# Kernel tuning notes

Measured on AMD Instinct MI355X. Metric: run time of the kernel, lower is better.

## Reference

```python
import jax, jax.numpy as jnp
import numpy as np

N = 50000
E = 800000
F_IN = 256
F_OUT = 128
ALPHA = 0.2  # leaky relu negative slope


def setup_inputs() -> dict:
    key = jax.random.key(0)
    k1, k2, k3, k4 = jax.random.split(key, 4)
    x = jax.random.normal(k1, (N, F_IN), dtype=jnp.float32)
    edge_index = jax.random.randint(k2, (2, E), 0, N, dtype=jnp.int64 if jax.config.jax_enable_x64 else jnp.int32)
    # xavier_normal gain=1.414
    W = jax.random.normal(k3, (F_IN, F_OUT), dtype=jnp.float32) * (1.414 * np.sqrt(2.0 / (F_IN + F_OUT)))
    a = jax.random.normal(k4, (2 * F_OUT, 2 * F_OUT), dtype=jnp.float32) * (1.414 * np.sqrt(2.0 / (4 * F_OUT)))
    return {"x": x, "edge_index": edge_index, "W": W, "a": a}


def reference(x, edge_index, W, a):
    n = x.shape[0]
    src = edge_index[0]  # rows of sparse adj
    dst = edge_index[1]  # cols of sparse adj
    h = x @ W  # [N, F_out]
    hs = h[src]  # [E, F_out] gather
    hd = h[dst]  # [E, F_out] gather
    # att_type == 'mx':
    # (a @ edge_h).sum(0) == a.sum(0) @ edge_h where edge_h = cat(hs, hd).T
    asum = a.sum(0)  # [2*F_out]
    lin = hs @ asum[:F_OUT] + hd @ asum[F_OUT:]  # [E]
    conv = (hs * hd).sum(axis=1)  # [E]
    z = lin * jax.nn.sigmoid(conv)
    edge_e = jnp.exp(-jnp.where(z >= 0, z, ALPHA * z))  # exp(-leakyrelu(z))
    # sparse spmm: rowsum (a @ ones) and aggregate (a @ h); dropout p=0 (eval)
    e_rowsum = jax.ops.segment_sum(edge_e, src, num_segments=n) + 1e-8  # [N]
    h_prime = jax.ops.segment_sum(edge_e[:, None] * hd, src, num_segments=n)  # [N, F_out]
    h_prime = h_prime / e_rowsum[:, None]
    return jax.nn.elu(h_prime)  # concat=True
```

## Files before the change

### kernel.cpp

```cpp
#include <hip/hip_runtime.h>

#define NF_IN 256
#define NF 128
#define NEG_SLOPE 0.2f
#define BUCKET 64

typedef float f32x4 __attribute__((ext_vector_type(4)));
typedef __bf16 bf16x8 __attribute__((ext_vector_type(8)));
typedef short short8 __attribute__((ext_vector_type(8)));
typedef _Float16 half8 __attribute__((ext_vector_type(8)));

__device__ __forceinline__ short bf16_rtne(float f) {
    unsigned u = __float_as_uint(f);
    u += 0x7fffu + ((u >> 16) & 1u);
    return (short)(u >> 16);
}

__global__ __launch_bounds__(256) void stage_pre(const float* __restrict__ a,
                                                 const float* __restrict__ W,
                                                 float* __restrict__ av,
                                                 short* __restrict__ Wt) {
    const int tid = threadIdx.x;
    if (blockIdx.x < 8) {
        float s = 0.f;
        const int r0 = blockIdx.x * 32;
        for (int i = 0; i < 32; ++i) s += a[(size_t)(r0 + i) * (2 * NF) + tid];
        atomicAdd(&av[tid], s);
    } else {
        const int i = (blockIdx.x - 8) * 256 + tid;
        const int k = i >> 7, c = i & 127;
        const int t = k >> 5, lg = (k >> 3) & 3, e = k & 7;
        const int q = c >> 4, col = c & 15;
        const float w = W[i];
        const unsigned b = __float_as_uint(w);
        const int base = t * 8192 + q * 512 + lg * 128 + col * 8 + e;
        Wt[base] = (short)(b >> 16);
        Wt[base + 4096] = bf16_rtne(w - __uint_as_float(b & 0xffff0000u));
    }
}

__global__ __launch_bounds__(256) void stage_proj(const float* __restrict__ x,
                                                  const short* __restrict__ Wt,
                                                  const float* __restrict__ av,
                                                  _Float16* __restrict__ h16,
                                                  float* __restrict__ scs,
                                                  float* __restrict__ scd, int n) {
    __shared__ short bts[2][8192];

    const int tid = threadIdx.x;
    const int lane = tid & 63;
    const int wv = tid >> 6;
    const int l15 = lane & 15;
    const int lg = lane >> 4;
    const int rbase = blockIdx.x * 64 + wv * 16;

    int arow = rbase + l15;
    if (arow >= n) arow = n - 1;
    const float* xr = x + (size_t)arow * NF_IN + lg * 8;

    short8 ah[8], al[8];
    #pragma unroll
    for (int t = 0; t < 8; ++t) {
        const float4 u0 = *(const float4*)(xr + t * 32);
        const float4 u1 = *(const float4*)(xr + t * 32 + 4);
        const float xs[8] = {u0.x, u0.y, u0.z, u0.w, u1.x, u1.y, u1.z, u1.w};
        #pragma unroll
        for (int e = 0; e < 8; ++e) {
            const unsigned b = __float_as_uint(xs[e]);
            ah[t][e] = (short)(b >> 16);
            al[t][e] = bf16_rtne(xs[e] - __uint_as_float(b & 0xffff0000u));
        }
    }

    f32x4 acc[8];
    #pragma unroll
    for (int q = 0; q < 8; ++q) acc[q] = (f32x4){0.f, 0.f, 0.f, 0.f};

    #define STAGE(t_, b_)                                                        \
        do {                                                                     \
            const short* gt_ = Wt + (size_t)(t_) * 8192;                         \
            _Pragma("unroll")                                                    \
            for (int i_ = 0; i_ < 4; ++i_) {                                     \
                const int ch_ = wv * 256 + i_ * 64;                              \
                __builtin_amdgcn_global_load_lds(                                \
                    (const __attribute__((address_space(1))) void*)              \
                        (gt_ + (size_t)(ch_ + lane) * 8),                        \
                    (__attribute__((address_space(3))) void*)&bts[b_][ch_ * 8],  \
                    16, 0, 0);                                                   \
            }                                                                    \
        } while (0)

    STAGE(0, 0);

    #pragma unroll
    for (int t = 0; t < 8; ++t) {
        __syncthreads();
        if (t < 7) STAGE(t + 1, (t + 1) & 1);
        const short* Bs = &bts[t & 1][0];
        const int boff = lg * 128 + l15 * 8;
        const bf16x8 ahv = __builtin_bit_cast(bf16x8, ah[t]);
        const bf16x8 alv = __builtin_bit_cast(bf16x8, al[t]);
        #pragma unroll
        for (int q = 0; q < 8; ++q) {
            const short8 bh = *(const short8*)(Bs + q * 512 + boff);
            const short8 bl = *(const short8*)(Bs + 4096 + q * 512 + boff);
            const bf16x8 bhv = __builtin_bit_cast(bf16x8, bh);
            const bf16x8 blv = __builtin_bit_cast(bf16x8, bl);
            acc[q] = __builtin_amdgcn_mfma_f32_16x16x32_bf16(ahv, bhv, acc[q], 0, 0, 0);
            acc[q] = __builtin_amdgcn_mfma_f32_16x16x32_bf16(alv, bhv, acc[q], 0, 0, 0);
            acc[q] = __builtin_amdgcn_mfma_f32_16x16x32_bf16(ahv, blv, acc[q], 0, 0, 0);
        }
    }
    #undef STAGE

    float avA[8], avB[8];
    #pragma unroll
    for (int q = 0; q < 8; ++q) {
        avA[q] = av[q * 16 + l15];
        avB[q] = av[NF + q * 16 + l15];
    }

    #pragma unroll
    for (int r = 0; r < 4; ++r) {
        float ps = 0.f, pd = 0.f;
        #pragma unroll
        for (int q = 0; q < 8; ++q) {
            ps += acc[q][r] * avA[q];
            pd += acc[q][r] * avB[q];
        }
        #pragma unroll
        for (int m = 1; m <= 8; m <<= 1) {
            ps += __shfl_xor(ps, m, 64);
            pd += __shfl_xor(pd, m, 64);
        }
        const int row = rbase + lg * 4 + r;
        if (row < n) {
            _Float16* hp = h16 + (size_t)row * NF;
            #pragma unroll
            for (int q = 0; q < 8; ++q) hp[q * 16 + l15] = (_Float16)acc[q][r];
            if (l15 == 0) { scs[row] = ps; scd[row] = pd; }
        }
    }
}

__global__ __launch_bounds__(256) void stage_fill(const int4* __restrict__ sv,
                                                  const int4* __restrict__ dv,
                                                  int* __restrict__ deg,
                                                  int* __restrict__ nbr, int m4) {
    const int i = blockIdx.x * blockDim.x + threadIdx.x;
    if (i >= m4) return;
    const int4 s = sv[i];
    const int4 d = dv[i];
    int k;
    k = atomicAdd(deg + s.x, 1); if (k < BUCKET) nbr[(s.x << 6) + k] = d.x;
    k = atomicAdd(deg + s.y, 1); if (k < BUCKET) nbr[(s.y << 6) + k] = d.y;
    k = atomicAdd(deg + s.z, 1); if (k < BUCKET) nbr[(s.z << 6) + k] = d.z;
    k = atomicAdd(deg + s.w, 1); if (k < BUCKET) nbr[(s.w << 6) + k] = d.w;
}

__global__ __launch_bounds__(256) void stage_agg(const _Float16* __restrict__ h16,
                                                 const int* __restrict__ nbr,
                                                 const int* __restrict__ deg,
                                                 const float* __restrict__ scs,
                                                 const float* __restrict__ scd,
                                                 float* __restrict__ out, int n) {
    const int node = (blockIdx.x * blockDim.x + threadIdx.x) >> 6;
    if (node >= n) return;
    const int lane = threadIdx.x & 63;
    const int qq = lane & 7;
    const int sub = lane >> 3;

    const half8* hself = (const half8*)(h16 + (size_t)node * NF + qq * 16);
    const half8 s0 = hself[0];
    const half8 s1 = hself[1];
    float p[16];
    #pragma unroll
    for (int e = 0; e < 8; ++e) { p[e] = (float)s0[e]; p[8 + e] = (float)s1[e]; }

    const float lbase = scs[node];
    const int org = node << 6;
    int dg = deg[node];
    if (dg > BUCKET) dg = BUCKET;

    float t[16];
    #pragma unroll
    for (int e = 0; e < 16; ++e) t[e] = 0.f;
    float zsum = 0.f;

    if (dg > 0) {
        int cu = nbr[org + ((sub < dg) ? sub : 0)];
        float lcu = scd[cu];
        for (int j = 0; j < dg; j += 8) {
            int nx = 0;
            float lnx = 0.f;
            if (j + 8 < dg) {
                const int jj = j + 8 + sub;
                nx = nbr[org + ((jj < dg) ? jj : 0)];
                lnx = scd[nx];
            }
            const half8* hn = (const half8*)(h16 + (size_t)cu * NF + qq * 16);
            const half8 n0 = hn[0];
            const half8 n1 = hn[1];
            float qv[16];
            #pragma unroll
            for (int e = 0; e < 8; ++e) { qv[e] = (float)n0[e]; qv[8 + e] = (float)n1[e]; }

            float cv = 0.f;
            #pragma unroll
            for (int e = 0; e < 16; ++e) cv += p[e] * qv[e];
            #pragma unroll
            for (int m = 4; m >= 1; m >>= 1) cv += __shfl_xor(cv, m, 64);

            const float gate = 1.0f / (1.0f + __expf(-cv));
            const float zz = (lbase + lcu) * gate;
            const float zr = (zz >= 0.f) ? zz : NEG_SLOPE * zz;
            float wt = __expf(-zr);
            if (j + sub >= dg) wt = 0.f;

            #pragma unroll
            for (int e = 0; e < 16; ++e) t[e] += wt * qv[e];
            zsum += wt;

            cu = nx;
            lcu = lnx;
        }
    }

    #pragma unroll
    for (int m = 8; m <= 32; m <<= 1) {
        #pragma unroll
        for (int e = 0; e < 16; ++e) t[e] += __shfl_xor(t[e], m, 64);
        zsum += __shfl_xor(zsum, m, 64);
    }

    const float norm = 1.0f / (zsum + 1e-8f);
    float y0 = t[0], y1 = t[1];
    #pragma unroll
    for (int i = 1; i < 8; ++i) {
        if (sub == i) { y0 = t[2 * i]; y1 = t[2 * i + 1]; }
    }
    y0 *= norm; y1 *= norm;
    y0 = (y0 > 0.f) ? y0 : (__expf(y0) - 1.f);
    y1 = (y1 > 0.f) ? y1 : (__expf(y1) - 1.f);
    *(float2*)(out + (size_t)node * NF + qq * 16 + sub * 2) = make_float2(y0, y1);
}

extern "C" void kernel_launch(void* const* d_in, const int* in_sizes, int n_in,
                              void* d_out, int out_size, void* d_ws, size_t ws_size,
                              hipStream_t stream) {
    const float* x = (const float*)d_in[0];
    const int* ei = (const int*)d_in[1];
    const float* W = (const float*)d_in[2];
    const float* a = (const float*)d_in[3];
    float* out = (float*)d_out;

    const int n = in_sizes[0] / NF_IN;
    const int E = in_sizes[1] / 2;
    const int m4 = E / 4;
    const int* srcp = ei;
    const int* dstp = ei + E;

    char* w = (char*)d_ws;
    _Float16* h16 = (_Float16*)w; w += (size_t)n * NF * 2;
    float* scs = (float*)w;   w += (size_t)n * 4;
    float* scd = (float*)w;   w += (size_t)n * 4;
    float* av = (float*)w;    w += 256 * 4;
    int* deg = (int*)w;       w += (size_t)n * 4;
    int* nbr = (int*)w;       w += (size_t)n * BUCKET * 4;
    short* Wt = (short*)w;    w += (size_t)8 * 8192 * 2 * 2;

    hipMemsetAsync(av, 0, (256 + (size_t)n) * sizeof(int), stream);

    stage_pre<<<136, 256, 0, stream>>>(a, W, av, Wt);
    stage_proj<<<(n + 63) / 64, 256, 0, stream>>>(x, Wt, av, h16, scs, scd, n);
    stage_fill<<<(m4 + 255) / 256, 256, 0, stream>>>((const int4*)srcp, (const int4*)dstp,
                                                     deg, nbr, m4);
    stage_agg<<<((size_t)n * 64 + 255) / 256, 256, 0, stream>>>(h16, nbr, deg, scs, scd,
                                                                out, n);
}
```

Before: 201.3 us.

## Fuse projection and CSR fill, narrow neighbor indices, prefetch features, butterfly reduce

Merges the projection and bucket-fill kernels into one launch so the atomic fill blocks can overlap the projection blocks. Neighbor indices are stored as 16-bit values to halve bucket traffic, which assumes fewer than 65536 nodes. The aggregation loop now prefetches the next neighbor's feature row a step ahead. The final cross-lane reduction uses a butterfly transpose exchange that needs fewer shuffles than the full all-reduce plus select. In exchange, register pressure rises and the index width limits graph size.

Result: faster. 188.7 us (-6.3%).

```diff
diff --git a/kernel.cpp b/kernel.cpp
--- a/kernel.cpp
+++ b/kernel.cpp
@@ -39,13 +39,26 @@
     }
 }
 
-__global__ __launch_bounds__(256) void stage_proj(const float* __restrict__ x,
-                                                  const short* __restrict__ Wt,
-                                                  const float* __restrict__ av,
-                                                  _Float16* __restrict__ h16,
-                                                  float* __restrict__ scs,
-                                                  float* __restrict__ scd, int n) {
+__global__ __launch_bounds__(256) void stage_projfill(
+        const float* __restrict__ x, const short* __restrict__ Wt,
+        const float* __restrict__ av, _Float16* __restrict__ h16,
+        float* __restrict__ scs, float* __restrict__ scd, int n, int nProj,
+        const int4* __restrict__ sv, const int4* __restrict__ dv,
+        int* __restrict__ deg, unsigned short* __restrict__ nbr, int m4) {
     __shared__ short bts[2][8192];
+
+    if (blockIdx.x >= nProj) {
+        const int i = (blockIdx.x - nProj) * 256 + threadIdx.x;
+        if (i >= m4) return;
+        const int4 s = sv[i];
+        const int4 d = dv[i];
+        int k;
+        k = atomicAdd(deg + s.x, 1); if (k < BUCKET) nbr[(s.x << 6) + k] = (unsigned short)d.x;
+        k = atomicAdd(deg + s.y, 1); if (k < BUCKET) nbr[(s.y << 6) + k] = (unsigned short)d.y;
+        k = atomicAdd(deg + s.z, 1); if (k < BUCKET) nbr[(s.z << 6) + k] = (unsigned short)d.z;
+        k = atomicAdd(deg + s.w, 1); if (k < BUCKET) nbr[(s.w << 6) + k] = (unsigned short)d.w;
+        return;
+    }
 
     const int tid = threadIdx.x;
     const int lane = tid & 63;
@@ -143,23 +156,8 @@
     }
 }
 
-__global__ __launch_bounds__(256) void stage_fill(const int4* __restrict__ sv,
-                                                  const int4* __restrict__ dv,
-                                                  int* __restrict__ deg,
-                                                  int* __restrict__ nbr, int m4) {
-    const int i = blockIdx.x * blockDim.x + threadIdx.x;
-    if (i >= m4) return;
-    const int4 s = sv[i];
-    const int4 d = dv[i];
-    int k;
-    k = atomicAdd(deg + s.x, 1); if (k < BUCKET) nbr[(s.x << 6) + k] = d.x;
-    k = atomicAdd(deg + s.y, 1); if (k < BUCKET) nbr[(s.y << 6) + k] = d.y;
-    k = atomicAdd(deg + s.z, 1); if (k < BUCKET) nbr[(s.z << 6) + k] = d.z;
-    k = atomicAdd(deg + s.w, 1); if (k < BUCKET) nbr[(s.w << 6) + k] = d.w;
-}
-
 __global__ __launch_bounds__(256) void stage_agg(const _Float16* __restrict__ h16,
-                                                 const int* __restrict__ nbr,
+                                                 const unsigned short* __restrict__ nbr,
                                                  const int* __restrict__ deg,
                                                  const float* __restrict__ scs,
                                                  const float* __restrict__ scd,
@@ -171,11 +169,11 @@
     const int sub = lane >> 3;
 
     const half8* hself = (const half8*)(h16 + (size_t)node * NF + qq * 16);
-    const half8 s0 = hself[0];
-    const half8 s1 = hself[1];
+    const half8 s0v = hself[0];
+    const half8 s1v = hself[1];
     float p[16];
     #pragma unroll
-    for (int e = 0; e < 8; ++e) { p[e] = (float)s0[e]; p[8 + e] = (float)s1[e]; }
+    for (int e = 0; e < 8; ++e) { p[e] = (float)s0v[e]; p[8 + e] = (float)s1v[e]; }
 
     const float lbase = scs[node];
     const int org = node << 6;
@@ -190,20 +188,25 @@
     if (dg > 0) {
         int cu = nbr[org + ((sub < dg) ? sub : 0)];
         float lcu = scd[cu];
+        const half8* hc = (const half8*)(h16 + (size_t)cu * NF + qq * 16);
+        half8 c0 = hc[0];
+        half8 c1 = hc[1];
         for (int j = 0; j < dg; j += 8) {
             int nx = 0;
             float lnx = 0.f;
+            half8 x0 = c0, x1 = c1;
             if (j + 8 < dg) {
                 const int jj = j + 8 + sub;
                 nx = nbr[org + ((jj < dg) ? jj : 0)];
                 lnx = scd[nx];
+                const half8* hx = (const half8*)(h16 + (size_t)nx * NF + qq * 16);
+                x0 = hx[0];
+                x1 = hx[1];
             }
-            const half8* hn = (const half8*)(h16 + (size_t)cu * NF + qq * 16);
-            const half8 n0 = hn[0];
-            const half8 n1 = hn[1];
+
             float qv[16];
             #pragma unroll
-            for (int e = 0; e < 8; ++e) { qv[e] = (float)n0[e]; qv[8 + e] = (float)n1[e]; }
+            for (int e = 0; e < 8; ++e) { qv[e] = (float)c0[e]; qv[8 + e] = (float)c1[e]; }
 
             float cv = 0.f;
             #pragma unroll
@@ -223,23 +226,47 @@
 
             cu = nx;
             lcu = lnx;
-        }
-    }
-
-    #pragma unroll
-    for (int m = 8; m <= 32; m <<= 1) {
-        #pragma unroll
-        for (int e = 0; e < 16; ++e) t[e] += __shfl_xor(t[e], m, 64);
-        zsum += __shfl_xor(zsum, m, 64);
+            c0 = x0;
+            c1 = x1;
+        }
+    }
+
+    #pragma unroll
+    for (int m = 8; m <= 32; m <<= 1) zsum += __shfl_xor(zsum, m, 64);
+
+    const int b0 = sub & 1, b1 = (sub >> 1) & 1, b2 = (sub >> 2) & 1;
+    float u[8];
+    #pragma unroll
+    for (int i = 0; i < 8; ++i) {
+        const int alo = ((i >> 1) << 2) | (i & 1);
+        const float ka = t[alo], kb = t[alo + 2];
+        const float keep = b0 ? kb : ka;
+        const float send = b0 ? ka : kb;
+        u[i] = keep + __shfl_xor(send, 8, 64);
+    }
+    float v[4];
+    #pragma unroll
+    for (int j = 0; j < 4; ++j) {
+        const int alo = ((j >> 1) << 2) | (j & 1);
+        const float ka = u[alo], kb = u[alo + 2];
+        const float keep = b1 ? kb : ka;
+        const float send = b1 ? ka : kb;
+        v[j] = keep + __shfl_xor(send, 16, 64);
+    }
+    float w0, w1;
+    {
+        const float ka = v[0], kb = v[2];
+        const float keep = b2 ? kb : ka, send = b2 ? ka : kb;
+        w0 = keep + __shfl_xor(send, 32, 64);
+    }
+    {
+        const float ka = v[1], kb = v[3];
+        const float keep = b2 ? kb : ka, send = b2 ? ka : kb;
+        w1 = keep + __shfl_xor(send, 32, 64);
     }
 
     const float norm = 1.0f / (zsum + 1e-8f);
-    float y0 = t[0], y1 = t[1];
-    #pragma unroll
-    for (int i = 1; i < 8; ++i) {
-        if (sub == i) { y0 = t[2 * i]; y1 = t[2 * i + 1]; }
-    }
-    y0 *= norm; y1 *= norm;
+    float y0 = w0 * norm, y1 = w1 * norm;
     y0 = (y0 > 0.f) ? y0 : (__expf(y0) - 1.f);
     y1 = (y1 > 0.f) ? y1 : (__expf(y1) - 1.f);
     *(float2*)(out + (size_t)node * NF + qq * 16 + sub * 2) = make_float2(y0, y1);
@@ -266,15 +293,18 @@
     float* scd = (float*)w;   w += (size_t)n * 4;
     float* av = (float*)w;    w += 256 * 4;
     int* deg = (int*)w;       w += (size_t)n * 4;
-    int* nbr = (int*)w;       w += (size_t)n * BUCKET * 4;
+    unsigned short* nbr = (unsigned short*)w; w += (size_t)n * BUCKET * 2;
     short* Wt = (short*)w;    w += (size_t)8 * 8192 * 2 * 2;
 
     hipMemsetAsync(av, 0, (256 + (size_t)n) * sizeof(int), stream);
 
+    const int nProj = (n + 63) / 64;
+    const int nFill = (m4 + 255) / 256;
+
     stage_pre<<<136, 256, 0, stream>>>(a, W, av, Wt);
-    stage_proj<<<(n + 63) / 64, 256, 0, stream>>>(x, Wt, av, h16, scs, scd, n);
-    stage_fill<<<(m4 + 255) / 256, 256, 0, stream>>>((const int4*)srcp, (const int4*)dstp,
-                                                     deg, nbr, m4);
+    stage_projfill<<<nProj + nFill, 256, 0, stream>>>(
+        x, Wt, av, h16, scs, scd, n, nProj,
+        (const int4*)srcp, (const int4*)dstp, deg, nbr, m4);
     stage_agg<<<((size_t)n * 64 + 255) / 256, 256, 0, stream>>>(h16, nbr, deg, scs, scd,
                                                                 out, n);
 }
```
